# Kernel optimization log

Hardware: AMD Instinct MI355X
Metric: run time of the kernel (lower is better)

Reference implementation:

```python
import jax, jax.numpy as jnp
import numpy as np

B, LAYERS, L, D = 16, 13, 512, 1024
MAX_WORDS = 256  # each word spans 2 contiguous BPE tokens


def setup_inputs() -> dict:
    key = jax.random.key(0)
    k1, k2 = jax.random.split(key)
    bpe_features = jax.random.normal(k1, (B, LAYERS, L, D), dtype=jnp.float32)
    layer_w = jax.random.normal(k2, (LAYERS,), dtype=jnp.float32)
    # contiguous alignment: word j covers BPE positions [2j, 2j+1]
    word_ids = jnp.broadcast_to(jnp.arange(L, dtype=jnp.int32) // 2, (B, L))
    return {"bpe_features": bpe_features, "layer_w": layer_w, "word_ids": word_ids}


def reference(bpe_features, layer_w, word_ids):
    # layer attention: softmax over per-layer scalar weights, weighted sum over layers
    w = jax.nn.softmax(layer_w)                          # [LAYERS]
    feats = jnp.einsum('l,blnd->bnd', w, bpe_features)   # [B, L, D]

    # bpe_mean: mean-pool BPE features into word features (fused segment reduce)
    def seg_mean(f, ids):
        s = jax.ops.segment_sum(f, ids, num_segments=MAX_WORDS)          # [W, D]
        c = jax.ops.segment_sum(jnp.ones((f.shape[0],), f.dtype), ids,
                                num_segments=MAX_WORDS)                  # [W]
        return s / jnp.maximum(c, 1.0)[:, None]

    return jax.vmap(seg_mean)(feats, word_ids)           # [B, MAX_WORDS, D]
```

## Files before the change

kernel.cpp:

```cpp
#include <hip/hip_runtime.h>

#define BB 16
#define LAYERS 13
#define LL 512
#define DD 1024
#define WW 256
#define WPB 4
#define TPB (2*WPB)
#define GPB (WW/WPB)

typedef float f32x4 __attribute__((ext_vector_type(4)));

__global__ __launch_bounds__(256) void MorphologicalTagger_13657996001460_kernel(
    const float* __restrict__ bpe,
    const float* __restrict__ layer_w,
    const int*   __restrict__ word_ids,
    float*       __restrict__ out)
{
    const int blk = blockIdx.x;
    const int b   = blk >> 6;
    const int jg  = blk & (GPB - 1);
    const int j0  = jg * WPB;
    const int tid = threadIdx.x;

    float w[LAYERS];
    float m = -3.402823e38f;
#pragma unroll
    for (int l = 0; l < LAYERS; ++l) {
        w[l] = layer_w[l];
        m = fmaxf(m, w[l]);
    }
    float s = 0.f;
#pragma unroll
    for (int l = 0; l < LAYERS; ++l) {
        w[l] = __expf(w[l] - m);
        s += w[l];
    }
    const float invs = 1.f / s;

    const int t0 = 2 * j0;
    float sc[TPB];
#pragma unroll
    for (int k = 0; k < TPB; ++k) {
        const int j = j0 + (k >> 1);
        sc[k] = (word_ids[b * LL + t0 + k] == j) ? 1.f : 0.f;
    }

    const int D4 = DD / 4;
    const f32x4* base =
        (const f32x4*)bpe + ((size_t)(b * LAYERS) * LL + (size_t)t0) * D4 + tid;
    const size_t lstride = (size_t)LL * D4;

    f32x4 acc[TPB];
#pragma unroll
    for (int k = 0; k < TPB; ++k) acc[k] = (f32x4)0.f;

#pragma unroll
    for (int l = 0; l < LAYERS; ++l) {
        const f32x4* pl = base + (size_t)l * lstride;
#pragma unroll
        for (int k = 0; k < TPB; ++k) {
            f32x4 x = pl[(size_t)k * D4];
            acc[k] += w[l] * x;
        }
    }

#pragma unroll
    for (int v = 0; v < WPB; ++v) {
        const float c = sc[2*v] + sc[2*v+1];
        const float r = invs / fmaxf(c, 1.f);
        f32x4 res = (sc[2*v] * r) * acc[2*v] + (sc[2*v+1] * r) * acc[2*v+1];
        f32x4* op = (f32x4*)out + ((size_t)b * WW + (size_t)(j0 + v)) * D4 + tid;
        __builtin_nontemporal_store(res, op);
    }
}

extern "C" void kernel_launch(void* const* d_in, const int* in_sizes, int n_in,
                              void* d_out, int out_size, void* d_ws, size_t ws_size,
                              hipStream_t stream) {
    const float* bpe      = (const float*)d_in[0];
    const float* layer_w  = (const float*)d_in[1];
    const int*   word_ids = (const int*)d_in[2];
    float* out = (float*)d_out;

    dim3 grid(BB * GPB);
    dim3 block(256);
    MorphologicalTagger_13657996001460_kernel<<<grid, block, 0, stream>>>(
        bpe, layer_w, word_ids, out);
}
```

Before: 561.6 us.

## Split layer reduction into two kernels via per-layer partials in workspace

Adds a two-phase path. Phase 1 launches one block per (batch, layer, word group), so each block reads a single layer, pools token pairs and writes per-layer partials to the workspace. Phase 2 sums the 13 partials per word and applies the mean. The goal is more parallelism (13x more blocks in the read-heavy phase), at the cost of writing and re-reading a partial buffer about half the input size plus an extra launch. The path only runs if the workspace is large enough; otherwise it falls back to the fused kernel.

```diff
diff --git a/kernel.cpp b/kernel.cpp
--- a/kernel.cpp
+++ b/kernel.cpp
@@ -5,25 +5,16 @@
 #define LL 512
 #define DD 1024
 #define WW 256
-#define WPB 4
-#define TPB (2*WPB)
-#define GPB (WW/WPB)
+#define D4 (DD/4)
 
 typedef float f32x4 __attribute__((ext_vector_type(4)));
 
-__global__ __launch_bounds__(256) void MorphologicalTagger_13657996001460_kernel(
-    const float* __restrict__ bpe,
-    const float* __restrict__ layer_w,
-    const int*   __restrict__ word_ids,
-    float*       __restrict__ out)
-{
-    const int blk = blockIdx.x;
-    const int b   = blk >> 6;
-    const int jg  = blk & (GPB - 1);
-    const int j0  = jg * WPB;
-    const int tid = threadIdx.x;
 
-    float w[LAYERS];
+#define JP 4
+#define GPB (WW/JP)
+
+__device__ __forceinline__ float softmax_invs(const float* __restrict__ layer_w,
+                                              float* w) {
     float m = -3.402823e38f;
 #pragma unroll
     for (int l = 0; l < LAYERS; ++l) {
@@ -36,37 +27,121 @@
         w[l] = __expf(w[l] - m);
         s += w[l];
     }
-    const float invs = 1.f / s;
+    return 1.f / s;
+}
+
+__global__ __launch_bounds__(256) void MorphologicalTagger_13657996001460_phase1(
+    const float* __restrict__ bpe,
+    const float* __restrict__ layer_w,
+    const int*   __restrict__ word_ids,
+    float*       __restrict__ partial)
+{
+    const int blk = blockIdx.x;
+    const int jg  = blk & (GPB - 1);
+    const int bl  = blk >> 6;
+    const int l   = bl % LAYERS;
+    const int b   = bl / LAYERS;
+    const int j0  = jg * JP;
+    const int t0  = 2 * j0;
+    const int tid = threadIdx.x;
+
+    float w[LAYERS];
+    const float invs = softmax_invs(layer_w, w);
+    const float wl = invs * w[l];
+
+    float sc[2 * JP];
+#pragma unroll
+    for (int k = 0; k < 2 * JP; ++k) {
+        const int j = j0 + (k >> 1);
+        sc[k] = (word_ids[b * LL + t0 + k] == j) ? wl : 0.f;
+    }
+
+    const f32x4* in =
+        (const f32x4*)bpe + ((size_t)(b * LAYERS + l) * LL + (size_t)t0) * D4 + tid;
+    f32x4* po = (f32x4*)partial +
+        ((size_t)(b * WW + j0) * LAYERS + (size_t)l) * D4 + tid;
+
+#pragma unroll
+    for (int v = 0; v < JP; ++v) {
+        f32x4 x0 = __builtin_nontemporal_load(in + (size_t)(2 * v) * D4);
+        f32x4 x1 = __builtin_nontemporal_load(in + (size_t)(2 * v + 1) * D4);
+        f32x4 p  = sc[2 * v] * x0 + sc[2 * v + 1] * x1;
+        po[(size_t)v * LAYERS * D4] = p;
+    }
+}
+
+__global__ __launch_bounds__(256) void MorphologicalTagger_13657996001460_phase2(
+    const float* __restrict__ partial,
+    const int*   __restrict__ word_ids,
+    float*       __restrict__ out)
+{
+    const int blk = blockIdx.x;
+    const int b   = blk >> 6;
+    const int jg  = blk & (GPB - 1);
+    const int j0  = jg * JP;
+    const int tid = threadIdx.x;
+
+#pragma unroll
+    for (int v = 0; v < JP; ++v) {
+        const int j = j0 + v;
+        const bool i0 = (word_ids[b * LL + 2 * j]     == j);
+        const bool i1 = (word_ids[b * LL + 2 * j + 1] == j);
+        const float cnt = (i0 ? 1.f : 0.f) + (i1 ? 1.f : 0.f);
+        const float r   = 1.f / fmaxf(cnt, 1.f);
+
+        const f32x4* pp = (const f32x4*)partial +
+            ((size_t)(b * WW + j) * LAYERS) * D4 + tid;
+        f32x4 acc = (f32x4)0.f;
+#pragma unroll
+        for (int l = 0; l < LAYERS; ++l)
+            acc += pp[(size_t)l * D4];
+
+        f32x4* op = (f32x4*)out + ((size_t)(b * WW + j)) * D4 + tid;
+        __builtin_nontemporal_store(acc * r, op);
+    }
+}
+
+__global__ __launch_bounds__(256) void MorphologicalTagger_13657996001460_kernel(
+    const float* __restrict__ bpe,
+    const float* __restrict__ layer_w,
+    const int*   __restrict__ word_ids,
+    float*       __restrict__ out)
+{
+    const int blk = blockIdx.x;
+    const int b   = blk >> 6;
+    const int jg  = blk & (GPB - 1);
+    const int j0  = jg * JP;
+    const int tid = threadIdx.x;
+
+    float w[LAYERS];
+    const float invs = softmax_invs(layer_w, w);
 
     const int t0 = 2 * j0;
-    float sc[TPB];
+    float sc[2 * JP];
 #pragma unroll
-    for (int k = 0; k < TPB; ++k) {
+    for (int k = 0; k < 2 * JP; ++k) {
         const int j = j0 + (k >> 1);
         sc[k] = (word_ids[b * LL + t0 + k] == j) ? 1.f : 0.f;
     }
 
-    const int D4 = DD / 4;
     const f32x4* base =
         (const f32x4*)bpe + ((size_t)(b * LAYERS) * LL + (size_t)t0) * D4 + tid;
     const size_t lstride = (size_t)LL * D4;
 
-    f32x4 acc[TPB];
+    f32x4 acc[2 * JP];
 #pragma unroll
-    for (int k = 0; k < TPB; ++k) acc[k] = (f32x4)0.f;
+    for (int k = 0; k < 2 * JP; ++k) acc[k] = (f32x4)0.f;
 
 #pragma unroll
     for (int l = 0; l < LAYERS; ++l) {
         const f32x4* pl = base + (size_t)l * lstride;
 #pragma unroll
-        for (int k = 0; k < TPB; ++k) {
-            f32x4 x = pl[(size_t)k * D4];
-            acc[k] += w[l] * x;
-        }
+        for (int k = 0; k < 2 * JP; ++k)
+            acc[k] += w[l] * pl[(size_t)k * D4];
     }
 
 #pragma unroll
-    for (int v = 0; v < WPB; ++v) {
+    for (int v = 0; v < JP; ++v) {
         const float c = sc[2*v] + sc[2*v+1];
         const float r = invs / fmaxf(c, 1.f);
         f32x4 res = (sc[2*v] * r) * acc[2*v] + (sc[2*v+1] * r) * acc[2*v+1];
@@ -83,8 +158,21 @@
     const int*   word_ids = (const int*)d_in[2];
     float* out = (float*)d_out;
 
-    dim3 grid(BB * GPB);
-    dim3 block(256);
-    MorphologicalTagger_13657996001460_kernel<<<grid, block, 0, stream>>>(
-        bpe, layer_w, word_ids, out);
+    const size_t need = (size_t)BB * WW * LAYERS * DD * sizeof(float);
+
+    if (d_ws != nullptr && ws_size >= need) {
+        float* partial = (float*)d_ws;
+        dim3 block(256);
+        dim3 g1(BB * LAYERS * GPB);
+        MorphologicalTagger_13657996001460_phase1<<<g1, block, 0, stream>>>(
+            bpe, layer_w, word_ids, partial);
+        dim3 g2(BB * GPB);
+        MorphologicalTagger_13657996001460_phase2<<<g2, block, 0, stream>>>(
+            partial, word_ids, out);
+    } else {
+        dim3 grid(BB * GPB);
+        dim3 block(256);
+        MorphologicalTagger_13657996001460_kernel<<<grid, block, 0, stream>>>(
+            bpe, layer_w, word_ids, out);
+    }
 }
```

Measured after the change: 602.0 us. 7.2% more time.
